# Kernel optimization log

Measured on AMD Instinct MI355X. Metric: run time of the kernel, lower is better.

The kernel has to match this reference:

```python
import jax, jax.numpy as jnp
import numpy as np

CACHE_LEN = 1024
EPS = 1e-5

def layer_norm(x, g, b):
    m = jnp.mean(x, axis=-1, keepdims=True)
    var = jnp.mean(jnp.square(x - m), axis=-1, keepdims=True)
    return (x - m) * jax.lax.rsqrt(var + EPS) * g + b

def setup_inputs() -> dict:
    key = jax.random.key(0)
    ks = jax.random.split(key, 16)
    B, Lq, Lk, D_IN, D_OUT = 4, 4096, 5119, 512, 512
    s = 1.0 / np.sqrt(D_IN)
    return {
        "q": jax.random.normal(ks[0], (B, Lq, D_IN), jnp.float32),
        "k": jax.random.normal(ks[1], (B, Lk, D_IN), jnp.float32),
        "v": jax.random.normal(ks[2], (B, Lk, D_IN), jnp.float32),
        "gq": jnp.ones((D_IN,), jnp.float32),
        "bq": jnp.zeros((D_IN,), jnp.float32),
        "gk": jnp.ones((D_IN,), jnp.float32),
        "bk": jnp.zeros((D_IN,), jnp.float32),
        "gv": jnp.ones((D_IN,), jnp.float32),
        "bv": jnp.zeros((D_IN,), jnp.float32),
        "Wq": jax.random.uniform(ks[3], (D_IN, D_OUT), jnp.float32, -s, s),
        "bwq": jax.random.uniform(ks[4], (D_OUT,), jnp.float32, -s, s),
        "Wk": jax.random.uniform(ks[5], (D_IN, D_OUT), jnp.float32, -s, s),
        "bwk": jax.random.uniform(ks[6], (D_OUT,), jnp.float32, -s, s),
        "Wv": jax.random.uniform(ks[7], (D_IN, D_OUT), jnp.float32, -s, s),
        "bwv": jax.random.uniform(ks[8], (D_OUT,), jnp.float32, -s, s),
    }

def reference(q, k, v, gq, bq, gk, bk, gv, bv, Wq, bwq, Wk, bwk, Wv, bwv):
    B, Lq, _ = q.shape
    Lk = k.shape[1]
    qp = layer_norm(q, gq, bq) @ Wq + bwq            # [B,Lq,Do]
    kp = layer_norm(k, gk, bk) @ Wk + bwk            # [B,Lk,Do]
    vp = layer_norm(v, gv, bv) @ Wv + bwv            # [B,Lk,Do]
    kv = jax.nn.relu(kp) * vp                         # [B,Lk,Do]
    # integrate3 skew-pad builds a banded ones mask: query row i attends to
    # kv columns [sup+i, sup+i+cache_len-1]. Equivalent sliding-window sum
    # computed via prefix sums (O(Lk*d) instead of O(Lq*Lk*d)).
    sup = Lk - Lq - CACHE_LEN + 1
    cs = jnp.cumsum(kv, axis=1)
    cs = jnp.concatenate([jnp.zeros_like(cs[:, :1]), cs], axis=1)  # [B,Lk+1,Do]
    starts = sup + jnp.arange(Lq)
    weighted = cs[:, starts + CACHE_LEN] - cs[:, starts]            # [B,Lq,Do]
    return jax.nn.relu(qp) * weighted
```

## Files before the change

### kernel.cpp

```cpp
#include <hip/hip_runtime.h>

#define B     4
#define LQ    4096
#define LK    5119
#define D     512
#define CACHE 1024
#define MQ    (B * LQ)
#define MK    (B * LK)
#define MKP   20480
#define NCH   160
#define TI    32

typedef float  f32x4  __attribute__((ext_vector_type(4)));
typedef __bf16 bf16x2 __attribute__((ext_vector_type(2)));
typedef __bf16 bf16x4 __attribute__((ext_vector_type(4)));
typedef __bf16 bf16x8 __attribute__((ext_vector_type(8)));

__device__ __forceinline__ void async16(void* lds, const void* g)
{
    __builtin_amdgcn_global_load_lds(
        (__attribute__((address_space(1))) void*)(g),
        (__attribute__((address_space(3))) void*)(lds),
        16, 0, 0);
}

__global__ __launch_bounds__(256) void ln_kernel(
    const float* __restrict__ q, const float* __restrict__ k,
    const float* __restrict__ v,
    const float* __restrict__ gq, const float* __restrict__ bq,
    const float* __restrict__ gk, const float* __restrict__ bk,
    const float* __restrict__ gv, const float* __restrict__ bv,
    __bf16* __restrict__ qn, __bf16* __restrict__ kn, __bf16* __restrict__ vn)
{
    const int z = blockIdx.y;
    const float *x, *g, *bb; __bf16* o; int M;
    if (z == 0)      { x = q; g = gq; bb = bq; o = qn; M = MQ; }
    else if (z == 1) { x = k; g = gk; bb = bk; o = kn; M = MK; }
    else             { x = v; g = gv; bb = bv; o = vn; M = MK; }
    const int r = blockIdx.x * 8 + (threadIdx.x >> 5);
    if (r >= M) return;

    const int c0 = (threadIdx.x & 31) * 16;
    const float* xr = x + (long)r * D + c0;

    float4 a[4];
#pragma unroll
    for (int j = 0; j < 4; ++j)
        a[j] = *reinterpret_cast<const float4*>(xr + j * 4);

    float s = 0.f, ss = 0.f;
#pragma unroll
    for (int j = 0; j < 4; ++j) {
        s  += a[j].x + a[j].y + a[j].z + a[j].w;
        ss += a[j].x*a[j].x + a[j].y*a[j].y + a[j].z*a[j].z + a[j].w*a[j].w;
    }
#pragma unroll
    for (int m = 1; m <= 16; m <<= 1) {
        s  += __shfl_xor(s,  m, 64);
        ss += __shfl_xor(ss, m, 64);
    }
    const float mean = s * (1.f / (float)D);
    const float var  = ss * (1.f / (float)D) - mean * mean;
    const float rs   = rsqrtf(var + 1e-5f);

    bf16x8 o0, o1;
#pragma unroll
    for (int j = 0; j < 4; ++j) {
        const float4 gv4 = *reinterpret_cast<const float4*>(g  + c0 + j * 4);
        const float4 bv4 = *reinterpret_cast<const float4*>(bb + c0 + j * 4);
        const float y0 = (a[j].x - mean) * rs * gv4.x + bv4.x;
        const float y1 = (a[j].y - mean) * rs * gv4.y + bv4.y;
        const float y2 = (a[j].z - mean) * rs * gv4.z + bv4.z;
        const float y3 = (a[j].w - mean) * rs * gv4.w + bv4.w;
        if (j < 2) {
            o0[j*4+0] = (__bf16)y0; o0[j*4+1] = (__bf16)y1;
            o0[j*4+2] = (__bf16)y2; o0[j*4+3] = (__bf16)y3;
        } else {
            o1[(j-2)*4+0] = (__bf16)y0; o1[(j-2)*4+1] = (__bf16)y1;
            o1[(j-2)*4+2] = (__bf16)y2; o1[(j-2)*4+3] = (__bf16)y3;
        }
    }
    __bf16* orow = o + (long)r * D + c0;
    *reinterpret_cast<bf16x8*>(orow)     = o0;
    *reinterpret_cast<bf16x8*>(orow + 8) = o1;
}

__global__ __launch_bounds__(256) void wconv_kernel(
    const float* __restrict__ Wq, const float* __restrict__ Wk,
    const float* __restrict__ Wv,
    __bf16* __restrict__ wtq, __bf16* __restrict__ wtk, __bf16* __restrict__ wtv)
{
    const int z = blockIdx.z;
    const float* W = (z == 0) ? Wq : (z == 1) ? Wk : Wv;
    __bf16*     Wt = (z == 0) ? wtq : (z == 1) ? wtk : wtv;
    const int n  = blockIdx.x * 256 + threadIdx.x;
    const int k0 = blockIdx.y * 8;
    bf16x8 o;
#pragma unroll
    for (int j = 0; j < 8; ++j)
        o[j] = (__bf16)W[(long)(k0 + j) * D + n];
    *reinterpret_cast<bf16x8*>(Wt + (long)n * D + k0) = o;
}

__global__ __launch_bounds__(256, 2) void gemm_q_kernel(
    const __bf16* __restrict__ A, const __bf16* __restrict__ Wt,
    const float* __restrict__ bias, __bf16* __restrict__ Cout)
{
    __shared__ __attribute__((aligned(16))) __bf16 As[128 * 64];
    __shared__ __attribute__((aligned(16))) __bf16 Bs[128 * 64];

    const int tid  = threadIdx.x;
    const int lane = tid & 63;
    const int wave = tid >> 6;
    const int quad = lane >> 4;
    const int l16  = lane & 15;
    const int wm   = wave >> 1;
    const int wn   = wave & 1;

    f32x4 acc[4][4];
#pragma unroll
    for (int i = 0; i < 4; ++i)
#pragma unroll
        for (int j = 0; j < 4; ++j)
            acc[i][j] = (f32x4){0.f, 0.f, 0.f, 0.f};

    const long arow0 = (long)blockIdx.x * 128;
    const long brow0 = (long)blockIdx.y * 128;
    const int  lrow  = lane >> 3;
    const int  lcs   = ((lane & 7) ^ lrow) * 8;

    for (int k0 = 0; k0 < D; k0 += 64) {
#pragma unroll
        for (int j = 0; j < 4; ++j) {
            const int r0  = (j * 4 + wave) * 8;
            const int row = r0 + lrow;
            async16(&As[r0 * 64], &A [(arow0 + row) * D + k0 + lcs]);
            async16(&Bs[r0 * 64], &Wt[(brow0 + row) * D + k0 + lcs]);
        }
        __syncthreads();

        bf16x8 af[4][2], bf[4][2];
#pragma unroll
        for (int tm = 0; tm < 4; ++tm) {
            const int m = wm * 64 + tm * 16 + l16;
#pragma unroll
            for (int kh = 0; kh < 2; ++kh)
                af[tm][kh] = *reinterpret_cast<const bf16x8*>(
                    &As[m * 64 + (((kh * 4 + quad) ^ (m & 7)) * 8)]);
        }
#pragma unroll
        for (int tn = 0; tn < 4; ++tn) {
            const int n = wn * 64 + tn * 16 + l16;
#pragma unroll
            for (int kh = 0; kh < 2; ++kh)
                bf[tn][kh] = *reinterpret_cast<const bf16x8*>(
                    &Bs[n * 64 + (((kh * 4 + quad) ^ (n & 7)) * 8)]);
        }

#pragma unroll
        for (int kh = 0; kh < 2; ++kh)
#pragma unroll
            for (int tm = 0; tm < 4; ++tm)
#pragma unroll
                for (int tn = 0; tn < 4; ++tn)
                    acc[tm][tn] = __builtin_amdgcn_mfma_f32_16x16x32_bf16(
                        af[tm][kh], bf[tn][kh], acc[tm][tn], 0, 0, 0);
        __syncthreads();
    }

#pragma unroll
    for (int tm = 0; tm < 4; ++tm) {
        const long row0 = arow0 + wm * 64 + tm * 16 + quad * 4;
#pragma unroll
        for (int tn = 0; tn < 4; ++tn) {
            const int col = (int)brow0 + wn * 64 + tn * 16 + l16;
            const float bv = bias[col];
#pragma unroll
            for (int r = 0; r < 4; ++r)
                Cout[(row0 + r) * D + col] =
                    (__bf16)fmaxf(acc[tm][tn][r] + bv, 0.f);
        }
    }
}

__global__ __launch_bounds__(256, 2) void gemm_kv_kernel(
    const __bf16* __restrict__ Ak, const __bf16* __restrict__ Av,
    const __bf16* __restrict__ Wtk, const __bf16* __restrict__ Wtv,
    const float* __restrict__ bk, const float* __restrict__ bv,
    __bf16* __restrict__ kvout)
{
    __shared__ __attribute__((aligned(16))) __bf16 Ks [128 * 64];
    __shared__ __attribute__((aligned(16))) __bf16 Vs [128 * 64];
    __shared__ __attribute__((aligned(16))) __bf16 WKs[64 * 64];
    __shared__ __attribute__((aligned(16))) __bf16 WVs[64 * 64];

    const int tid  = threadIdx.x;
    const int lane = tid & 63;
    const int wave = tid >> 6;
    const int quad = lane >> 4;
    const int l16  = lane & 15;
    const int wm   = wave >> 1;
    const int wn   = wave & 1;

    f32x4 acck[4][2], accv[4][2];
#pragma unroll
    for (int i = 0; i < 4; ++i)
#pragma unroll
        for (int j = 0; j < 2; ++j) {
            acck[i][j] = (f32x4){0.f, 0.f, 0.f, 0.f};
            accv[i][j] = (f32x4){0.f, 0.f, 0.f, 0.f};
        }

    const long arow0 = (long)blockIdx.x * 128;
    const long brow0 = (long)blockIdx.y * 64;
    const int  lrow  = lane >> 3;
    const int  lcs   = ((lane & 7) ^ lrow) * 8;

    for (int k0 = 0; k0 < D; k0 += 64) {
#pragma unroll
        for (int j = 0; j < 4; ++j) {
            const int r0  = (j * 4 + wave) * 8;
            const int row = r0 + lrow;
            async16(&Ks[r0 * 64], &Ak[(arow0 + row) * D + k0 + lcs]);
            async16(&Vs[r0 * 64], &Av[(arow0 + row) * D + k0 + lcs]);
        }
#pragma unroll
        for (int j = 0; j < 2; ++j) {
            const int r0  = (j * 4 + wave) * 8;
            const int row = r0 + lrow;
            async16(&WKs[r0 * 64], &Wtk[(brow0 + row) * D + k0 + lcs]);
            async16(&WVs[r0 * 64], &Wtv[(brow0 + row) * D + k0 + lcs]);
        }
        __syncthreads();

        bf16x8 fa[4][2], fb[2][2];
#pragma unroll
        for (int tm = 0; tm < 4; ++tm) {
            const int m = wm * 64 + tm * 16 + l16;
#pragma unroll
            for (int kh = 0; kh < 2; ++kh)
                fa[tm][kh] = *reinterpret_cast<const bf16x8*>(
                    &Ks[m * 64 + (((kh * 4 + quad) ^ (m & 7)) * 8)]);
        }
#pragma unroll
        for (int tn = 0; tn < 2; ++tn) {
            const int n = wn * 32 + tn * 16 + l16;
#pragma unroll
            for (int kh = 0; kh < 2; ++kh)
                fb[tn][kh] = *reinterpret_cast<const bf16x8*>(
                    &WKs[n * 64 + (((kh * 4 + quad) ^ (n & 7)) * 8)]);
        }
#pragma unroll
        for (int kh = 0; kh < 2; ++kh)
#pragma unroll
            for (int tm = 0; tm < 4; ++tm)
#pragma unroll
                for (int tn = 0; tn < 2; ++tn)
                    acck[tm][tn] = __builtin_amdgcn_mfma_f32_16x16x32_bf16(
                        fa[tm][kh], fb[tn][kh], acck[tm][tn], 0, 0, 0);
#pragma unroll
        for (int tm = 0; tm < 4; ++tm) {
            const int m = wm * 64 + tm * 16 + l16;
#pragma unroll
            for (int kh = 0; kh < 2; ++kh)
                fa[tm][kh] = *reinterpret_cast<const bf16x8*>(
                    &Vs[m * 64 + (((kh * 4 + quad) ^ (m & 7)) * 8)]);
        }
#pragma unroll
        for (int tn = 0; tn < 2; ++tn) {
            const int n = wn * 32 + tn * 16 + l16;
#pragma unroll
            for (int kh = 0; kh < 2; ++kh)
                fb[tn][kh] = *reinterpret_cast<const bf16x8*>(
                    &WVs[n * 64 + (((kh * 4 + quad) ^ (n & 7)) * 8)]);
        }
#pragma unroll
        for (int kh = 0; kh < 2; ++kh)
#pragma unroll
            for (int tm = 0; tm < 4; ++tm)
#pragma unroll
                for (int tn = 0; tn < 2; ++tn)
                    accv[tm][tn] = __builtin_amdgcn_mfma_f32_16x16x32_bf16(
                        fa[tm][kh], fb[tn][kh], accv[tm][tn], 0, 0, 0);
        __syncthreads();
    }

#pragma unroll
    for (int tm = 0; tm < 4; ++tm) {
        const long row0 = arow0 + wm * 64 + tm * 16 + quad * 4;
#pragma unroll
        for (int tn = 0; tn < 2; ++tn) {
            const int col = (int)brow0 + wn * 32 + tn * 16 + l16;
            const float bkc = bk[col];
            const float bvc = bv[col];
#pragma unroll
            for (int r = 0; r < 4; ++r) {
                const float kp = fmaxf(acck[tm][tn][r] + bkc, 0.f);
                const float vp = accv[tm][tn][r] + bvc;
                kvout[(row0 + r) * D + col] = (__bf16)(kp * vp);
            }
        }
    }
}

__global__ __launch_bounds__(256) void chunk_kernel(
    const __bf16* __restrict__ kv, float* __restrict__ Csum)
{
    const int c    = blockIdx.x;
    const int b    = blockIdx.y;
    const int col2 = threadIdx.x * 2;
    const __bf16* base = kv + ((long)b * LK + (long)c * 32) * D + col2;
    float s0 = 0.f, s1 = 0.f;
#pragma unroll
    for (int j = 0; j < 32; ++j) {
        const bf16x2 vv = *reinterpret_cast<const bf16x2*>(base + (long)j * D);
        s0 += (float)vv[0];
        s1 += (float)vv[1];
    }
    float* o = Csum + ((long)b * NCH + c) * D + col2;
    o[0] = s0; o[1] = s1;
}

__global__ __launch_bounds__(256) void window_kernel(
    const __bf16* __restrict__ kv, const float* __restrict__ Csum,
    const __bf16* __restrict__ qpb, float* __restrict__ out)
{
    const int iq   = blockIdx.x;
    const int b    = blockIdx.y;
    const int i0   = iq * TI;
    const int col2 = threadIdx.x * 2;

    const float* cs = Csum + (long)b * NCH * D + col2;
    float s0 = 0.f, s1 = 0.f;
#pragma unroll
    for (int c = 0; c < 32; ++c) {
        const float2 cv = *reinterpret_cast<const float2*>(cs + (long)(iq + c) * D);
        s0 += cv.x; s1 += cv.y;
    }

    const __bf16* kvb = kv  + (long)b * LK * D + col2;
    const __bf16* qb  = qpb + (long)b * LQ * D + col2;
    float*        ob  = out + (long)b * LQ * D + col2;

#pragma unroll 8
    for (int i = i0; i < i0 + TI; ++i) {
        const bf16x2 qv = *reinterpret_cast<const bf16x2*>(qb + (long)i * D);
        *reinterpret_cast<float2*>(ob + (long)i * D) =
            make_float2((float)qv[0] * s0, (float)qv[1] * s1);
        const bf16x2 lead  = *reinterpret_cast<const bf16x2*>(kvb + (long)(i + CACHE) * D);
        const bf16x2 trail = *reinterpret_cast<const bf16x2*>(kvb + (long)i * D);
        s0 += (float)lead[0] - (float)trail[0];
        s1 += (float)lead[1] - (float)trail[1];
    }
}

extern "C" void kernel_launch(void* const* d_in, const int* in_sizes, int n_in,
                              void* d_out, int out_size, void* d_ws, size_t ws_size,
                              hipStream_t stream)
{
    const float* q   = (const float*)d_in[0];
    const float* k   = (const float*)d_in[1];
    const float* v   = (const float*)d_in[2];
    const float* gq  = (const float*)d_in[3];
    const float* bq  = (const float*)d_in[4];
    const float* gk  = (const float*)d_in[5];
    const float* bk  = (const float*)d_in[6];
    const float* gv  = (const float*)d_in[7];
    const float* bv  = (const float*)d_in[8];
    const float* Wq  = (const float*)d_in[9];
    const float* bwq = (const float*)d_in[10];
    const float* Wk  = (const float*)d_in[11];
    const float* bwk = (const float*)d_in[12];
    const float* Wv  = (const float*)d_in[13];
    const float* bwv = (const float*)d_in[14];
    float* out = (float*)d_out;

    char* ws = (char*)d_ws;
    __bf16* qn   = (__bf16*)ws;
    __bf16* kn   = qn  + (long)MQ  * D;
    __bf16* vn   = kn  + (long)MKP * D;
    __bf16* qpb  = vn  + (long)MKP * D;
    __bf16* kvb  = qpb + (long)MQ  * D;
    __bf16* wtq  = kvb + (long)MKP * D;
    __bf16* wtk  = wtq + (long)D * D;
    __bf16* wtv  = wtk + (long)D * D;
    float*  Csum = (float*)(wtv + (long)D * D);

    ln_kernel<<<dim3(2560, 3), 256, 0, stream>>>(q, k, v, gq, bq, gk, bk, gv, bv,
                                                 qn, kn, vn);
    wconv_kernel<<<dim3(2, 64, 3), 256, 0, stream>>>(Wq, Wk, Wv, wtq, wtk, wtv);

    gemm_q_kernel<<<dim3(MQ / 128, D / 128), 256, 0, stream>>>(qn, wtq, bwq, qpb);

    gemm_kv_kernel<<<dim3(MKP / 128, D / 64), 256, 0, stream>>>(
        kn, vn, wtk, wtv, bwk, bwv, kvb);

    chunk_kernel<<<dim3(NCH, B), 256, 0, stream>>>(kvb, Csum);

    window_kernel<<<dim3(LQ / TI, B), 256, 0, stream>>>(kvb, Csum, qpb, out);
}
```

Baseline: 237.9 us.

## Merge prep kernels, fuse Q and KV GEMMs, compute chunk sums in epilogue

Folds the weight-conversion kernel into the layernorm kernel as an extra grid slice. Merges the Q GEMM and the KV GEMM into one launch and pads each batch's K/V rows to 5120 so the 32-row chunk sums can be computed in the KV GEMM epilogue via shuffles, which removes the separate chunk kernel. This cuts the launch count from six to three and drops one read pass over kv. In exchange the fused GEMM kernel carries the larger LDS footprint for all blocks and adds epilogue reduction work.

```diff
diff --git a/kernel.cpp b/kernel.cpp
--- a/kernel.cpp
+++ b/kernel.cpp
@@ -3,17 +3,16 @@
 #define B     4
 #define LQ    4096
 #define LK    5119
+#define LKP   5120
 #define D     512
 #define CACHE 1024
 #define MQ    (B * LQ)
-#define MK    (B * LK)
-#define MKP   20480
+#define MKP   (B * LKP)
 #define NCH   160
 #define TI    32
 
 typedef float  f32x4  __attribute__((ext_vector_type(4)));
 typedef __bf16 bf16x2 __attribute__((ext_vector_type(2)));
-typedef __bf16 bf16x4 __attribute__((ext_vector_type(4)));
 typedef __bf16 bf16x8 __attribute__((ext_vector_type(8)));
 
 __device__ __forceinline__ void async16(void* lds, const void* g)
@@ -24,24 +23,55 @@
         16, 0, 0);
 }
 
-__global__ __launch_bounds__(256) void ln_kernel(
+__global__ __launch_bounds__(256) void prep_kernel(
     const float* __restrict__ q, const float* __restrict__ k,
     const float* __restrict__ v,
     const float* __restrict__ gq, const float* __restrict__ bq,
     const float* __restrict__ gk, const float* __restrict__ bk,
     const float* __restrict__ gv, const float* __restrict__ bv,
-    __bf16* __restrict__ qn, __bf16* __restrict__ kn, __bf16* __restrict__ vn)
+    const float* __restrict__ Wq, const float* __restrict__ Wk,
+    const float* __restrict__ Wv,
+    __bf16* __restrict__ qn, __bf16* __restrict__ kn, __bf16* __restrict__ vn,
+    __bf16* __restrict__ wtq, __bf16* __restrict__ wtk, __bf16* __restrict__ wtv)
 {
     const int z = blockIdx.y;
-    const float *x, *g, *bb; __bf16* o; int M;
-    if (z == 0)      { x = q; g = gq; bb = bq; o = qn; M = MQ; }
-    else if (z == 1) { x = k; g = gk; bb = bk; o = kn; M = MK; }
-    else             { x = v; g = gv; bb = bv; o = vn; M = MK; }
-    const int r = blockIdx.x * 8 + (threadIdx.x >> 5);
-    if (r >= M) return;
+
+    if (z == 3) {
+        const int idx = blockIdx.x;
+        if (idx >= 384) return;
+        const int zz  = idx >> 7;
+        const int rem = idx & 127;
+        const float* W = (zz == 0) ? Wq : (zz == 1) ? Wk : Wv;
+        __bf16*     Wt = (zz == 0) ? wtq : (zz == 1) ? wtk : wtv;
+        const int n  = (rem & 1) * 256 + threadIdx.x;
+        const int k0 = (rem >> 1) * 8;
+        bf16x8 o;
+#pragma unroll
+        for (int j = 0; j < 8; ++j)
+            o[j] = (__bf16)W[(long)(k0 + j) * D + n];
+        *reinterpret_cast<bf16x8*>(Wt + (long)n * D + k0) = o;
+        return;
+    }
+
+    const float *x, *g, *bb; __bf16* o;
+    if (z == 0)      { x = q; g = gq; bb = bq; o = qn; }
+    else if (z == 1) { x = k; g = gk; bb = bk; o = kn; }
+    else             { x = v; g = gv; bb = bv; o = vn; }
+
+    const int rp = blockIdx.x * 8 + (threadIdx.x >> 5);
+    long rin;
+    if (z == 0) {
+        if (rp >= MQ) return;
+        rin = rp;
+    } else {
+        const int bch = rp / LKP;
+        const int i   = rp - bch * LKP;
+        if (i == LK) return;
+        rin = (long)bch * LK + i;
+    }
 
     const int c0 = (threadIdx.x & 31) * 16;
-    const float* xr = x + (long)r * D + c0;
+    const float* xr = x + rin * D + c0;
 
     float4 a[4];
 #pragma unroll
@@ -80,35 +110,24 @@
             o1[(j-2)*4+2] = (__bf16)y2; o1[(j-2)*4+3] = (__bf16)y3;
         }
     }
-    __bf16* orow = o + (long)r * D + c0;
+    __bf16* orow = o + (long)rp * D + c0;
     *reinterpret_cast<bf16x8*>(orow)     = o0;
     *reinterpret_cast<bf16x8*>(orow + 8) = o1;
 }
 
-__global__ __launch_bounds__(256) void wconv_kernel(
-    const float* __restrict__ Wq, const float* __restrict__ Wk,
-    const float* __restrict__ Wv,
-    __bf16* __restrict__ wtq, __bf16* __restrict__ wtk, __bf16* __restrict__ wtv)
+__global__ __launch_bounds__(256, 2) void gemm_fused_kernel(
+    const __bf16* __restrict__ qn, const __bf16* __restrict__ kn,
+    const __bf16* __restrict__ vn,
+    const __bf16* __restrict__ wtq, const __bf16* __restrict__ wtk,
+    const __bf16* __restrict__ wtv,
+    const float* __restrict__ bwq, const float* __restrict__ bwk,
+    const float* __restrict__ bwv,
+    __bf16* __restrict__ qpb, __bf16* __restrict__ kvb,
+    float* __restrict__ Csum)
 {
-    const int z = blockIdx.z;
-    const float* W = (z == 0) ? Wq : (z == 1) ? Wk : Wv;
-    __bf16*     Wt = (z == 0) ? wtq : (z == 1) ? wtk : wtv;
-    const int n  = blockIdx.x * 256 + threadIdx.x;
-    const int k0 = blockIdx.y * 8;
-    bf16x8 o;
-#pragma unroll
-    for (int j = 0; j < 8; ++j)
-        o[j] = (__bf16)W[(long)(k0 + j) * D + n];
-    *reinterpret_cast<bf16x8*>(Wt + (long)n * D + k0) = o;
-}
-
-__global__ __launch_bounds__(256, 2) void gemm_q_kernel(
-    const __bf16* __restrict__ A, const __bf16* __restrict__ Wt,
-    const float* __restrict__ bias, __bf16* __restrict__ Cout)
-{
-    __shared__ __attribute__((aligned(16))) __bf16 As[128 * 64];
-    __shared__ __attribute__((aligned(16))) __bf16 Bs[128 * 64];
-
+    __shared__ __attribute__((aligned(16))) __bf16 smem[24576];
+
+    const int bid  = blockIdx.x;
     const int tid  = threadIdx.x;
     const int lane = tid & 63;
     const int wave = tid >> 6;
@@ -116,209 +135,200 @@
     const int l16  = lane & 15;
     const int wm   = wave >> 1;
     const int wn   = wave & 1;
-
-    f32x4 acc[4][4];
-#pragma unroll
-    for (int i = 0; i < 4; ++i)
-#pragma unroll
-        for (int j = 0; j < 4; ++j)
-            acc[i][j] = (f32x4){0.f, 0.f, 0.f, 0.f};
-
-    const long arow0 = (long)blockIdx.x * 128;
-    const long brow0 = (long)blockIdx.y * 128;
-    const int  lrow  = lane >> 3;
-    const int  lcs   = ((lane & 7) ^ lrow) * 8;
-
-    for (int k0 = 0; k0 < D; k0 += 64) {
-#pragma unroll
-        for (int j = 0; j < 4; ++j) {
-            const int r0  = (j * 4 + wave) * 8;
-            const int row = r0 + lrow;
-            async16(&As[r0 * 64], &A [(arow0 + row) * D + k0 + lcs]);
-            async16(&Bs[r0 * 64], &Wt[(brow0 + row) * D + k0 + lcs]);
+    const int lrow = lane >> 3;
+    const int lcs  = ((lane & 7) ^ lrow) * 8;
+
+    if (bid < 512) {
+        __bf16* As = smem;
+        __bf16* Bs = smem + 8192;
+
+        f32x4 acc[4][4];
+#pragma unroll
+        for (int i = 0; i < 4; ++i)
+#pragma unroll
+            for (int j = 0; j < 4; ++j)
+                acc[i][j] = (f32x4){0.f, 0.f, 0.f, 0.f};
+
+        const long arow0 = (long)(bid >> 2) * 128;
+        const long brow0 = (long)(bid & 3) * 128;
+
+        for (int k0 = 0; k0 < D; k0 += 64) {
+#pragma unroll
+            for (int j = 0; j < 4; ++j) {
+                const int r0  = (j * 4 + wave) * 8;
+                const int row = r0 + lrow;
+                async16(&As[r0 * 64], &qn [(arow0 + row) * D + k0 + lcs]);
+                async16(&Bs[r0 * 64], &wtq[(brow0 + row) * D + k0 + lcs]);
+            }
+            __syncthreads();
+
+            bf16x8 af[4][2], bf[4][2];
+#pragma unroll
+            for (int tm = 0; tm < 4; ++tm) {
+                const int m = wm * 64 + tm * 16 + l16;
+#pragma unroll
+                for (int kh = 0; kh < 2; ++kh)
+                    af[tm][kh] = *reinterpret_cast<const bf16x8*>(
+                        &As[m * 64 + (((kh * 4 + quad) ^ (m & 7)) * 8)]);
+            }
+#pragma unroll
+            for (int tn = 0; tn < 4; ++tn) {
+                const int n = wn * 64 + tn * 16 + l16;
+#pragma unroll
+                for (int kh = 0; kh < 2; ++kh)
+                    bf[tn][kh] = *reinterpret_cast<const bf16x8*>(
+                        &Bs[n * 64 + (((kh * 4 + quad) ^ (n & 7)) * 8)]);
+            }
+#pragma unroll
+            for (int kh = 0; kh < 2; ++kh)
+#pragma unroll
+                for (int tm = 0; tm < 4; ++tm)
+#pragma unroll
+                    for (int tn = 0; tn < 4; ++tn)
+                        acc[tm][tn] = __builtin_amdgcn_mfma_f32_16x16x32_bf16(
+                            af[tm][kh], bf[tn][kh], acc[tm][tn], 0, 0, 0);
+            __syncthreads();
         }
-        __syncthreads();
-
-        bf16x8 af[4][2], bf[4][2];
+
 #pragma unroll
         for (int tm = 0; tm < 4; ++tm) {
-            const int m = wm * 64 + tm * 16 + l16;
+            const long row0 = arow0 + wm * 64 + tm * 16 + quad * 4;
+#pragma unroll
+            for (int tn = 0; tn < 4; ++tn) {
+                const int col = (int)brow0 + wn * 64 + tn * 16 + l16;
+                const float bv = bwq[col];
+#pragma unroll
+                for (int r = 0; r < 4; ++r)
+                    qpb[(row0 + r) * D + col] =
+                        (__bf16)fmaxf(acc[tm][tn][r] + bv, 0.f);
+            }
+        }
+    } else {
+        __bf16* Ks  = smem;
+        __bf16* Vs  = smem + 8192;
+        __bf16* WKs = smem + 16384;
+        __bf16* WVs = smem + 20480;
+
+        const int bid2  = bid - 512;
+        const int ntile = bid2 / 160;
+        const int mtile = bid2 - ntile * 160;
+
+        f32x4 acck[4][2], accv[4][2];
+#pragma unroll
+        for (int i = 0; i < 4; ++i)
+#pragma unroll
+            for (int j = 0; j < 2; ++j) {
+                acck[i][j] = (f32x4){0.f, 0.f, 0.f, 0.f};
+                accv[i][j] = (f32x4){0.f, 0.f, 0.f, 0.f};
+            }
+
+        const long arow0 = (long)mtile * 128;
+        const long brow0 = (long)ntile * 64;
+
+        for (int k0 = 0; k0 < D; k0 += 64) {
+#pragma unroll
+            for (int j = 0; j < 4; ++j) {
+                const int r0  = (j * 4 + wave) * 8;
+                const int row = r0 + lrow;
+                async16(&Ks[r0 * 64], &kn[(arow0 + row) * D + k0 + lcs]);
+                async16(&Vs[r0 * 64], &vn[(arow0 + row) * D + k0 + lcs]);
+            }
+#pragma unroll
+            for (int j = 0; j < 2; ++j) {
+                const int r0  = (j * 4 + wave) * 8;
+                const int row = r0 + lrow;
+                async16(&WKs[r0 * 64], &wtk[(brow0 + row) * D + k0 + lcs]);
+                async16(&WVs[r0 * 64], &wtv[(brow0 + row) * D + k0 + lcs]);
+            }
+            __syncthreads();
+
+            bf16x8 fa[4][2], fb[2][2];
+#pragma unroll
+            for (int tm = 0; tm < 4; ++tm) {
+                const int m = wm * 64 + tm * 16 + l16;
+#pragma unroll
+                for (int kh = 0; kh < 2; ++kh)
+                    fa[tm][kh] = *reinterpret_cast<const bf16x8*>(
+                        &Ks[m * 64 + (((kh * 4 + quad) ^ (m & 7)) * 8)]);
+            }
+#pragma unroll
+            for (int tn = 0; tn < 2; ++tn) {
+                const int n = wn * 32 + tn * 16 + l16;
+#pragma unroll
+                for (int kh = 0; kh < 2; ++kh)
+                    fb[tn][kh] = *reinterpret_cast<const bf16x8*>(
+                        &WKs[n * 64 + (((kh * 4 + quad) ^ (n & 7)) * 8)]);
+            }
 #pragma unroll
             for (int kh = 0; kh < 2; ++kh)
-                af[tm][kh] = *reinterpret_cast<const bf16x8*>(
-                    &As[m * 64 + (((kh * 4 + quad) ^ (m & 7)) * 8)]);
+#pragma unroll
+                for (int tm = 0; tm < 4; ++tm)
+#pragma unroll
+                    for (int tn = 0; tn < 2; ++tn)
+                        acck[tm][tn] = __builtin_amdgcn_mfma_f32_16x16x32_bf16(
+                            fa[tm][kh], fb[tn][kh], acck[tm][tn], 0, 0, 0);
+#pragma unroll
+            for (int tm = 0; tm < 4; ++tm) {
+                const int m = wm * 64 + tm * 16 + l16;
+#pragma unroll
+                for (int kh = 0; kh < 2; ++kh)
+                    fa[tm][kh] = *reinterpret_cast<const bf16x8*>(
+                        &Vs[m * 64 + (((kh * 4 + quad) ^ (m & 7)) * 8)]);
+            }
+#pragma unroll
+            for (int tn = 0; tn < 2; ++tn) {
+                const int n = wn * 32 + tn * 16 + l16;
+#pragma unroll
+                for (int kh = 0; kh < 2; ++kh)
+                    fb[tn][kh] = *reinterpret_cast<const bf16x8*>(
+                        &WVs[n * 64 + (((kh * 4 + quad) ^ (n & 7)) * 8)]);
+            }
+#pragma unroll
+            for (int kh = 0; kh < 2; ++kh)
+#pragma unroll
+                for (int tm = 0; tm < 4; ++tm)
+#pragma unroll
+                    for (int tn = 0; tn < 2; ++tn)
+                        accv[tm][tn] = __builtin_amdgcn_mfma_f32_16x16x32_bf16(
+                            fa[tm][kh], fb[tn][kh], accv[tm][tn], 0, 0, 0);
+            __syncthreads();
         }
-#pragma unroll
-        for (int tn = 0; tn < 4; ++tn) {
-            const int n = wn * 64 + tn * 16 + l16;
-#pragma unroll
-            for (int kh = 0; kh < 2; ++kh)
-                bf[tn][kh] = *reinterpret_cast<const bf16x8*>(
-                    &Bs[n * 64 + (((kh * 4 + quad) ^ (n & 7)) * 8)]);
+
+        float part[2][2] = {{0.f, 0.f}, {0.f, 0.f}};
+#pragma unroll
+        for (int tm = 0; tm < 4; ++tm) {
+            const long row0 = arow0 + wm * 64 + tm * 16 + quad * 4;
+#pragma unroll
+            for (int tn = 0; tn < 2; ++tn) {
+                const int col = (int)brow0 + wn * 32 + tn * 16 + l16;
+                const float bkc = bwk[col];
+                const float bvc = bwv[col];
+#pragma unroll
+                for (int r = 0; r < 4; ++r) {
+                    const float kp = fmaxf(acck[tm][tn][r] + bkc, 0.f);
+                    const float vp = accv[tm][tn][r] + bvc;
+                    const __bf16 kb = (__bf16)(kp * vp);
+                    kvb[(row0 + r) * D + col] = kb;
+                    part[tn][tm >> 1] += (float)kb;
+                }
+            }
         }
-
-#pragma unroll
-        for (int kh = 0; kh < 2; ++kh)
-#pragma unroll
-            for (int tm = 0; tm < 4; ++tm)
-#pragma unroll
-                for (int tn = 0; tn < 4; ++tn)
-                    acc[tm][tn] = __builtin_amdgcn_mfma_f32_16x16x32_bf16(
-                        af[tm][kh], bf[tn][kh], acc[tm][tn], 0, 0, 0);
-        __syncthreads();
-    }
-
-#pragma unroll
-    for (int tm = 0; tm < 4; ++tm) {
-        const long row0 = arow0 + wm * 64 + tm * 16 + quad * 4;
-#pragma unroll
-        for (int tn = 0; tn < 4; ++tn) {
-            const int col = (int)brow0 + wn * 64 + tn * 16 + l16;
-            const float bv = bias[col];
-#pragma unroll
-            for (int r = 0; r < 4; ++r)
-                Cout[(row0 + r) * D + col] =
-                    (__bf16)fmaxf(acc[tm][tn][r] + bv, 0.f);
-        }
-    }
-}
-
-__global__ __launch_bounds__(256, 2) void gemm_kv_kernel(
-    const __bf16* __restrict__ Ak, const __bf16* __restrict__ Av,
-    const __bf16* __restrict__ Wtk, const __bf16* __restrict__ Wtv,
-    const float* __restrict__ bk, const float* __restrict__ bv,
-    __bf16* __restrict__ kvout)
-{
-    __shared__ __attribute__((aligned(16))) __bf16 Ks [128 * 64];
-    __shared__ __attribute__((aligned(16))) __bf16 Vs [128 * 64];
-    __shared__ __attribute__((aligned(16))) __bf16 WKs[64 * 64];
-    __shared__ __attribute__((aligned(16))) __bf16 WVs[64 * 64];
-
-    const int tid  = threadIdx.x;
-    const int lane = tid & 63;
-    const int wave = tid >> 6;
-    const int quad = lane >> 4;
-    const int l16  = lane & 15;
-    const int wm   = wave >> 1;
-    const int wn   = wave & 1;
-
-    f32x4 acck[4][2], accv[4][2];
-#pragma unroll
-    for (int i = 0; i < 4; ++i)
-#pragma unroll
-        for (int j = 0; j < 2; ++j) {
-            acck[i][j] = (f32x4){0.f, 0.f, 0.f, 0.f};
-            accv[i][j] = (f32x4){0.f, 0.f, 0.f, 0.f};
-        }
-
-    const long arow0 = (long)blockIdx.x * 128;
-    const long brow0 = (long)blockIdx.y * 64;
-    const int  lrow  = lane >> 3;
-    const int  lcs   = ((lane & 7) ^ lrow) * 8;
-
-    for (int k0 = 0; k0 < D; k0 += 64) {
-#pragma unroll
-        for (int j = 0; j < 4; ++j) {
-            const int r0  = (j * 4 + wave) * 8;
-            const int row = r0 + lrow;
-            async16(&Ks[r0 * 64], &Ak[(arow0 + row) * D + k0 + lcs]);
-            async16(&Vs[r0 * 64], &Av[(arow0 + row) * D + k0 + lcs]);
-        }
-#pragma unroll
-        for (int j = 0; j < 2; ++j) {
-            const int r0  = (j * 4 + wave) * 8;
-            const int row = r0 + lrow;
-            async16(&WKs[r0 * 64], &Wtk[(brow0 + row) * D + k0 + lcs]);
-            async16(&WVs[r0 * 64], &Wtv[(brow0 + row) * D + k0 + lcs]);
-        }
-        __syncthreads();
-
-        bf16x8 fa[4][2], fb[2][2];
-#pragma unroll
-        for (int tm = 0; tm < 4; ++tm) {
-            const int m = wm * 64 + tm * 16 + l16;
-#pragma unroll
-            for (int kh = 0; kh < 2; ++kh)
-                fa[tm][kh] = *reinterpret_cast<const bf16x8*>(
-                    &Ks[m * 64 + (((kh * 4 + quad) ^ (m & 7)) * 8)]);
-        }
-#pragma unroll
-        for (int tn = 0; tn < 2; ++tn) {
-            const int n = wn * 32 + tn * 16 + l16;
-#pragma unroll
-            for (int kh = 0; kh < 2; ++kh)
-                fb[tn][kh] = *reinterpret_cast<const bf16x8*>(
-                    &WKs[n * 64 + (((kh * 4 + quad) ^ (n & 7)) * 8)]);
-        }
-#pragma unroll
-        for (int kh = 0; kh < 2; ++kh)
-#pragma unroll
-            for (int tm = 0; tm < 4; ++tm)
-#pragma unroll
-                for (int tn = 0; tn < 2; ++tn)
-                    acck[tm][tn] = __builtin_amdgcn_mfma_f32_16x16x32_bf16(
-                        fa[tm][kh], fb[tn][kh], acck[tm][tn], 0, 0, 0);
-#pragma unroll
-        for (int tm = 0; tm < 4; ++tm) {
-            const int m = wm * 64 + tm * 16 + l16;
-#pragma unroll
-            for (int kh = 0; kh < 2; ++kh)
-                fa[tm][kh] = *reinterpret_cast<const bf16x8*>(
-                    &Vs[m * 64 + (((kh * 4 + quad) ^ (m & 7)) * 8)]);
-        }
-#pragma unroll
-        for (int tn = 0; tn < 2; ++tn) {
-            const int n = wn * 32 + tn * 16 + l16;
-#pragma unroll
-            for (int kh = 0; kh < 2; ++kh)
-                fb[tn][kh] = *reinterpret_cast<const bf16x8*>(
-                    &WVs[n * 64 + (((kh * 4 + quad) ^ (n & 7)) * 8)]);
-        }
-#pragma unroll
-        for (int kh = 0; kh < 2; ++kh)
-#pragma unroll
-            for (int tm = 0; tm < 4; ++tm)
-#pragma unroll
-                for (int tn = 0; tn < 2; ++tn)
-                    accv[tm][tn] = __builtin_amdgcn_mfma_f32_16x16x32_bf16(
-                        fa[tm][kh], fb[tn][kh], accv[tm][tn], 0, 0, 0);
-        __syncthreads();
-    }
-
-#pragma unroll
-    for (int tm = 0; tm < 4; ++tm) {
-        const long row0 = arow0 + wm * 64 + tm * 16 + quad * 4;
-#pragma unroll
-        for (int tn = 0; tn < 2; ++tn) {
-            const int col = (int)brow0 + wn * 32 + tn * 16 + l16;
-            const float bkc = bk[col];
-            const float bvc = bv[col];
-#pragma unroll
-            for (int r = 0; r < 4; ++r) {
-                const float kp = fmaxf(acck[tm][tn][r] + bkc, 0.f);
-                const float vp = accv[tm][tn][r] + bvc;
-                kvout[(row0 + r) * D + col] = (__bf16)(kp * vp);
-            }
-        }
-    }
-}
-
-__global__ __launch_bounds__(256) void chunk_kernel(
-    const __bf16* __restrict__ kv, float* __restrict__ Csum)
-{
-    const int c    = blockIdx.x;
-    const int b    = blockIdx.y;
-    const int col2 = threadIdx.x * 2;
-    const __bf16* base = kv + ((long)b * LK + (long)c * 32) * D + col2;
-    float s0 = 0.f, s1 = 0.f;
-#pragma unroll
-    for (int j = 0; j < 32; ++j) {
-        const bf16x2 vv = *reinterpret_cast<const bf16x2*>(base + (long)j * D);
-        s0 += (float)vv[0];
-        s1 += (float)vv[1];
-    }
-    float* o = Csum + ((long)b * NCH + c) * D + col2;
-    o[0] = s0; o[1] = s1;
+#pragma unroll
+        for (int tn = 0; tn < 2; ++tn)
+#pragma unroll
+            for (int th = 0; th < 2; ++th) {
+                float vv = part[tn][th];
+                vv += __shfl_xor(vv, 16, 64);
+                vv += __shfl_xor(vv, 32, 64);
+                if (quad == 0) {
+                    const int fc = ((int)(arow0 >> 5)) + wm * 2 + th;
+                    const int bb = fc / NCH;
+                    const int cc = fc - bb * NCH;
+                    const int col = (int)brow0 + wn * 32 + tn * 16 + l16;
+                    Csum[((long)bb * NCH + cc) * D + col] = vv;
+                }
+            }
+    }
 }
 
 __global__ __launch_bounds__(256) void window_kernel(
@@ -338,9 +348,9 @@
         s0 += cv.x; s1 += cv.y;
     }
 
-    const __bf16* kvb = kv  + (long)b * LK * D + col2;
-    const __bf16* qb  = qpb + (long)b * LQ * D + col2;
-    float*        ob  = out + (long)b * LQ * D + col2;
+    const __bf16* kvb = kv  + (long)b * LKP * D + col2;
+    const __bf16* qb  = qpb + (long)b * LQ  * D + col2;
+    float*        ob  = out + (long)b * LQ  * D + col2;
 
 #pragma unroll 8
     for (int i = i0; i < i0 + TI; ++i) {
@@ -386,16 +396,12 @@
     __bf16* wtv  = wtk + (long)D * D;
     float*  Csum = (float*)(wtv + (long)D * D);
 
-    ln_kernel<<<dim3(2560, 3), 256, 0, stream>>>(q, k, v, gq, bq, gk, bk, gv, bv,
-                                                 qn, kn, vn);
-    wconv_kernel<<<dim3(2, 64, 3), 256, 0, stream>>>(Wq, Wk, Wv, wtq, wtk, wtv);
-
-    gemm_q_kernel<<<dim3(MQ / 128, D / 128), 256, 0, stream>>>(qn, wtq, bwq, qpb);
-
-    gemm_kv_kernel<<<dim3(MKP / 128, D / 64), 256, 0, stream>>>(
-        kn, vn, wtk, wtv, bwk, bwv, kvb);
-
-    chunk_kernel<<<dim3(NCH, B), 256, 0, stream>>>(kvb, Csum);
+    prep_kernel<<<dim3(2560, 4), 256, 0, stream>>>(
+        q, k, v, gq, bq, gk, bk, gv, bv, Wq, Wk, Wv,
+        qn, kn, vn, wtq, wtk, wtv);
+
+    gemm_fused_kernel<<<512 + 1280, 256, 0, stream>>>(
+        qn, kn, vn, wtq, wtk, wtv, bwq, bwk, bwv, qpb, kvb, Csum);
 
     window_kernel<<<dim3(LQ / TI, B), 256, 0, stream>>>(kvb, Csum, qpb, out);
 }
```

Measured after the change: 235.7 us. No clear change (-0.9%).
